# Optimization experiments

Measured on AMD Instinct MI355X. Metric: run time of the kernel, lower is better.

The kernel has to match this reference:

```python
import jax, jax.numpy as jnp
import numpy as np

B, S, H = 16, 4096, 1024

def setup_inputs() -> dict:
    key = jax.random.key(0)
    k1, k2, k3 = jax.random.split(key, 3)
    lstm_output = jax.random.normal(k1, (B, S, H), dtype=jnp.float32)
    # nn.Linear(H, H): weight [H, H] (out, in), bias [H]
    W = jax.random.normal(k2, (H, H), dtype=jnp.float32) * (1.0 / np.sqrt(H))
    b = jax.random.normal(k3, (H,), dtype=jnp.float32) * 0.01
    return {"lstm_output": lstm_output, "W": W, "b": b}

def reference(lstm_output, W, b):
    # energy = tanh(x @ W^T + b)  [B, S, H]
    energy = jnp.tanh(jnp.einsum('bsh,oh->bso', lstm_output, W) + b)
    # softmax over the sequence dim (dim=1), per hidden channel
    scores = jax.nn.softmax(energy, axis=1)
    # weighted-sum pooling over sequence -> [B, H]
    context = jnp.sum(scores * lstm_output, axis=1)
    return context
```

## Files before the change

### kernel.cpp

```cpp
#include <hip/hip_runtime.h>
#include <hip/hip_bf16.h>

#define Bsz  16
#define Sdim 4096
#define Hdim 1024
#define Mtot (Bsz * Sdim)
#define Kdim Hdim
#define Ndim Hdim

#define BM2 256
#define BN2 256
#define BK2 32
#define MT2 (Mtot / BM2)
#define NT2 (Ndim / BN2)
#define NKT2 (Kdim / BK2)

#define BM 128
#define BN 128
#define BK 32
#define MT (Mtot / BM)
#define NT (Ndim / BN)
#define NKT (Kdim / BK)

typedef short s16x8 __attribute__((ext_vector_type(8)));
typedef float f32x4 __attribute__((ext_vector_type(4)));

__device__ __forceinline__ unsigned short f2bf(float f) {
  __hip_bfloat16 h = __float2bfloat16(f);
  unsigned short u;
  __builtin_memcpy(&u, &h, 2);
  return u;
}
__device__ __forceinline__ float bf2f(unsigned short u) {
  __hip_bfloat16 h;
  __builtin_memcpy(&h, &u, 2);
  return __bfloat162float(h);
}
__device__ __forceinline__ s16x8 cvt8(float4 u, float4 v) {
  s16x8 r;
  r[0] = (short)f2bf(u.x); r[1] = (short)f2bf(u.y);
  r[2] = (short)f2bf(u.z); r[3] = (short)f2bf(u.w);
  r[4] = (short)f2bf(v.x); r[5] = (short)f2bf(v.y);
  r[6] = (short)f2bf(v.z); r[7] = (short)f2bf(v.w);
  return r;
}

__device__ __forceinline__ void gload_lds16(const unsigned short* g, unsigned short* l) {
  __builtin_amdgcn_global_load_lds(
      (const __attribute__((address_space(1))) unsigned int*)g,
      (__attribute__((address_space(3))) unsigned int*)l,
      16, 0, 0);
}

__global__ __launch_bounds__(256) void xconv_kernel(const float* __restrict__ X,
                                                    unsigned short* __restrict__ Xb) {
  size_t i = (size_t)blockIdx.x * 256 + threadIdx.x;
  float4 u = reinterpret_cast<const float4*>(X)[2 * i];
  float4 v = reinterpret_cast<const float4*>(X)[2 * i + 1];
  reinterpret_cast<s16x8*>(Xb)[i] = cvt8(u, v);
}

__global__ __launch_bounds__(256) void wconv_kernel(const float* __restrict__ W,
                                                    unsigned short* __restrict__ Wb) {
  int i = blockIdx.x * 256 + threadIdx.x;
  float4 v = reinterpret_cast<const float4*>(W)[i];
  ushort4 o;
  o.x = f2bf(v.x); o.y = f2bf(v.y); o.z = f2bf(v.z); o.w = f2bf(v.w);
  reinterpret_cast<ushort4*>(Wb)[i] = o;
}

__global__ __launch_bounds__(512, 2) void attn_main(
    const unsigned short* __restrict__ Xb,
    const unsigned short* __restrict__ Wb,
    const float* __restrict__ bias,
    float* __restrict__ lpart,
    float* __restrict__ cpart) {
  __shared__ unsigned short Asl[4][BM2 * BK2];
  __shared__ unsigned short Bsl[4][BN2 * BK2];
  __shared__ float red[2][2][BN2];

  int bid = blockIdx.x;
  int swz = (bid & 7) * (MT2 * NT2 / 8) + (bid >> 3);
  const int mt = swz >> 2;
  const int nt = swz & 3;
  const int m0 = mt * BM2;
  const int n0 = nt * BN2;

  const int tid  = threadIdx.x;
  const int l    = tid & 63;
  const int w    = tid >> 6;
  const int wm   = w >> 2;
  const int wn   = w & 3;
  const int lr   = l & 15;
  const int lk   = l >> 4;

  f32x4 acc[8][4];
#pragma unroll
  for (int i = 0; i < 8; i++)
#pragma unroll
    for (int j = 0; j < 4; j++) acc[i][j] = (f32x4){0.f, 0.f, 0.f, 0.f};

  const int srow = w * 16 + (l >> 2);
  const int scol = (((l & 3) ^ ((l >> 3) & 3)) << 3);
  const unsigned short* srcA0 = Xb + (size_t)(m0 + srow) * Kdim + scol;
  const unsigned short* srcA1 = srcA0 + (size_t)128 * Kdim;
  const unsigned short* srcB0 = Wb + (size_t)(n0 + srow) * Kdim + scol;
  const unsigned short* srcB1 = srcB0 + (size_t)128 * Kdim;

  int offA[8], offB[4];
#pragma unroll
  for (int mr = 0; mr < 8; mr++) {
    const int r = wm * 128 + mr * 16 + lr;
    offA[mr] = r * BK2 + ((lk * 8) ^ (((r >> 1) & 3) << 3));
  }
#pragma unroll
  for (int n = 0; n < 4; n++) {
    const int rn = wn * 64 + n * 16 + lr;
    offB[n] = rn * BK2 + ((lk * 8) ^ (((rn >> 1) & 3) << 3));
  }

#pragma unroll
  for (int u = 0; u < 3; ++u) {
    unsigned short* dA = &Asl[u][w * 512];
    unsigned short* dB = &Bsl[u][w * 512];
    gload_lds16(srcA0 + u * BK2, dA);
    gload_lds16(srcA1 + u * BK2, dA + 4096);
    gload_lds16(srcB0 + u * BK2, dB);
    gload_lds16(srcB1 + u * BK2, dB + 4096);
  }

  for (int t = 0; t < NKT2; ++t) {
    if (t < NKT2 - 2)       asm volatile("s_waitcnt vmcnt(8)" ::: "memory");
    else if (t == NKT2 - 2) asm volatile("s_waitcnt vmcnt(4)" ::: "memory");
    else                    asm volatile("s_waitcnt vmcnt(0)" ::: "memory");
    __builtin_amdgcn_s_barrier();

    const int tp = t + 3;
    if (tp < NKT2) {
      unsigned short* dA = &Asl[tp & 3][w * 512];
      unsigned short* dB = &Bsl[tp & 3][w * 512];
      gload_lds16(srcA0 + tp * BK2, dA);
      gload_lds16(srcA1 + tp * BK2, dA + 4096);
      gload_lds16(srcB0 + tp * BK2, dB);
      gload_lds16(srcB1 + tp * BK2, dB + 4096);
    }
    asm volatile("" ::: "memory");

    const unsigned short* As = Asl[t & 3];
    const unsigned short* Bs = Bsl[t & 3];
    s16x8 af[8], bf[4];
#pragma unroll
    for (int j = 0; j < 8; ++j) af[j] = *(const s16x8*)&As[offA[j]];
#pragma unroll
    for (int n = 0; n < 4; ++n) bf[n] = *(const s16x8*)&Bs[offB[n]];
#pragma unroll
    for (int j = 0; j < 8; ++j)
#pragma unroll
      for (int n = 0; n < 4; ++n)
        acc[j][n] = __builtin_amdgcn_mfma_f32_16x16x32_bf16(af[j], bf[n], acc[j][n], 0, 0, 0);
  }

  float lsum[4], csum[4];
#pragma unroll
  for (int nr = 0; nr < 4; nr++) {
    const int o = n0 + wn * 64 + nr * 16 + lr;
    const float bv = bias[o];
    float lacc = 0.f, cacc = 0.f;
#pragma unroll
    for (int mr = 0; mr < 8; mr++) {
      const int sr = m0 + wm * 128 + mr * 16 + lk * 4;
#pragma unroll
      for (int r = 0; r < 4; r++) {
        float e  = acc[mr][nr][r] + bv;
        float t  = __expf(2.f * e);
        float th = 1.f - __fdividef(2.f, t + 1.f);
        float sc = __expf(th);
        float xv = bf2f(Xb[(size_t)(sr + r) * Kdim + o]);
        lacc += sc;
        cacc += sc * xv;
      }
    }
    lacc += __shfl_xor(lacc, 16); lacc += __shfl_xor(lacc, 32);
    cacc += __shfl_xor(cacc, 16); cacc += __shfl_xor(cacc, 32);
    lsum[nr] = lacc; csum[nr] = cacc;
  }

  if (lk == 0) {
#pragma unroll
    for (int nr = 0; nr < 4; nr++) {
      red[wm][0][wn * 64 + nr * 16 + lr] = lsum[nr];
      red[wm][1][wn * 64 + nr * 16 + lr] = csum[nr];
    }
  }
  __syncthreads();
  if (tid < BN2) {
    float L = red[0][0][tid] + red[1][0][tid];
    float C = red[0][1][tid] + red[1][1][tid];
    lpart[(size_t)mt * Ndim + n0 + tid] = L;
    cpart[(size_t)mt * Ndim + n0 + tid] = C;
  }
}

__global__ __launch_bounds__(256) void attn_main_fb(
    const float* __restrict__ X, const unsigned short* __restrict__ Wb,
    const float* __restrict__ bias, float* __restrict__ lpart, float* __restrict__ cpart) {
  __shared__ unsigned short Al[BM * BK];
  __shared__ unsigned short Bl[BN * BK];
  __shared__ float red[2][2][BN];
  int bid = blockIdx.x;
  int swz = (bid & 7) * (MT * NT / 8) + (bid >> 3);
  int mt = swz >> 3, nt = swz & 7;
  const int m0 = mt * BM, n0 = nt * BN;
  const int tid = threadIdx.x, lane = tid & 63, wave = tid >> 6;
  const int wm = wave >> 1, wn = wave & 1, lr = lane & 15, lk = lane >> 4;
  f32x4 acc[4][4];
#pragma unroll
  for (int i = 0; i < 4; i++)
#pragma unroll
    for (int j = 0; j < 4; j++) acc[i][j] = (f32x4){0.f, 0.f, 0.f, 0.f};
  const int srow_st = tid >> 1, scol_st = (tid & 1) * 16;
  const float*          Ag = X  + (size_t)(m0 + srow_st) * Kdim + scol_st;
  const unsigned short* Bg = Wb + (size_t)(n0 + srow_st) * Kdim + scol_st;
  float4 a0 = *(const float4*)(Ag + 0), a1 = *(const float4*)(Ag + 4);
  float4 a2 = *(const float4*)(Ag + 8), a3 = *(const float4*)(Ag + 12);
  s16x8 b0 = *(const s16x8*)(Bg + 0), b1 = *(const s16x8*)(Bg + 8);
  for (int kt = 0; kt < NKT; ++kt) {
    __syncthreads();
    *(s16x8*)&Al[srow_st * BK + scol_st]     = cvt8(a0, a1);
    *(s16x8*)&Al[srow_st * BK + scol_st + 8] = cvt8(a2, a3);
    *(s16x8*)&Bl[srow_st * BK + scol_st]     = b0;
    *(s16x8*)&Bl[srow_st * BK + scol_st + 8] = b1;
    __syncthreads();
    if (kt + 1 < NKT) {
      const float* ap = Ag + (kt + 1) * BK;
      a0 = *(const float4*)(ap);     a1 = *(const float4*)(ap + 4);
      a2 = *(const float4*)(ap + 8); a3 = *(const float4*)(ap + 12);
      const unsigned short* bp = Bg + (kt + 1) * BK;
      b0 = *(const s16x8*)(bp);      b1 = *(const s16x8*)(bp + 8);
    }
    s16x8 af[4], bfr[4];
#pragma unroll
    for (int mr = 0; mr < 4; mr++)
      af[mr] = *(const s16x8*)&Al[(wm * 64 + mr * 16 + lr) * BK + lk * 8];
#pragma unroll
    for (int nr = 0; nr < 4; nr++)
      bfr[nr] = *(const s16x8*)&Bl[(wn * 64 + nr * 16 + lr) * BK + lk * 8];
#pragma unroll
    for (int mr = 0; mr < 4; mr++)
#pragma unroll
      for (int nr = 0; nr < 4; nr++)
        acc[mr][nr] = __builtin_amdgcn_mfma_f32_16x16x32_bf16(af[mr], bfr[nr], acc[mr][nr], 0, 0, 0);
  }
  float lsum[4], csum[4];
#pragma unroll
  for (int nr = 0; nr < 4; nr++) {
    const int o = n0 + wn * 64 + nr * 16 + lr;
    const float bv = bias[o];
    float lacc = 0.f, cacc = 0.f;
#pragma unroll
    for (int mr = 0; mr < 4; mr++) {
      const int sr = m0 + wm * 64 + mr * 16 + lk * 4;
#pragma unroll
      for (int r = 0; r < 4; r++) {
        float e  = acc[mr][nr][r] + bv;
        float t  = __expf(2.f * e);
        float th = 1.f - __fdividef(2.f, t + 1.f);
        float sc = __expf(th);
        float xv = X[(size_t)(sr + r) * Kdim + o];
        lacc += sc; cacc += sc * xv;
      }
    }
    lacc += __shfl_xor(lacc, 16); lacc += __shfl_xor(lacc, 32);
    cacc += __shfl_xor(cacc, 16); cacc += __shfl_xor(cacc, 32);
    lsum[nr] = lacc; csum[nr] = cacc;
  }
  if (lk == 0) {
#pragma unroll
    for (int nr = 0; nr < 4; nr++) {
      red[wm][0][wn * 64 + nr * 16 + lr] = lsum[nr];
      red[wm][1][wn * 64 + nr * 16 + lr] = csum[nr];
    }
  }
  __syncthreads();
  if (tid < BN) {
    float L = red[0][0][tid] + red[1][0][tid];
    float C = red[0][1][tid] + red[1][1][tid];
    lpart[(size_t)mt * Ndim + n0 + tid] = L;
    cpart[(size_t)mt * Ndim + n0 + tid] = C;
  }
}

__global__ __launch_bounds__(256) void finalize_kernel(const float* __restrict__ lpart,
                                                       const float* __restrict__ cpart,
                                                       float* __restrict__ out, int chunks) {
  int i = blockIdx.x * 256 + threadIdx.x;
  int b = i >> 10, o = i & 1023;
  float L = 0.f, C = 0.f;
  for (int sc = 0; sc < chunks; ++sc) {
    size_t idx = (size_t)(b * chunks + sc) * Ndim + o;
    L += lpart[idx];
    C += cpart[idx];
  }
  out[i] = C / L;
}

extern "C" void kernel_launch(void* const* d_in, const int* in_sizes, int n_in,
                              void* d_out, int out_size, void* d_ws, size_t ws_size,
                              hipStream_t stream) {
  const float* X    = (const float*)d_in[0];
  const float* W    = (const float*)d_in[1];
  const float* bias = (const float*)d_in[2];
  float* out = (float*)d_out;

  const size_t xb_bytes = (size_t)Mtot * Kdim * 2;
  const size_t wb_bytes = (size_t)Ndim * Kdim * 2;
  const size_t lp_bytes = (size_t)MT * Ndim * 4;
  const size_t need = xb_bytes + wb_bytes + 2 * lp_bytes;

  if (ws_size >= need) {
    unsigned short* Xb = (unsigned short*)d_ws;
    unsigned short* Wb = (unsigned short*)((char*)d_ws + xb_bytes);
    float* lpart = (float*)((char*)d_ws + xb_bytes + wb_bytes);
    float* cpart = lpart + (size_t)MT2 * Ndim;
    xconv_kernel<<<dim3(Mtot * (Kdim / 8) / 256), dim3(256), 0, stream>>>(X, Xb);
    wconv_kernel<<<dim3(Ndim * Kdim / 1024), dim3(256), 0, stream>>>(W, Wb);
    attn_main<<<dim3(MT2 * NT2), dim3(512), 0, stream>>>(Xb, Wb, bias, lpart, cpart);
    finalize_kernel<<<dim3(Bsz * Hdim / 256), dim3(256), 0, stream>>>(lpart, cpart, out,
                                                                      Sdim / BM2);
  } else {
    unsigned short* Wb = (unsigned short*)d_ws;
    float* lpart = (float*)((char*)d_ws + wb_bytes);
    float* cpart = lpart + (size_t)MT * Ndim;
    wconv_kernel<<<dim3(Ndim * Kdim / 1024), dim3(256), 0, stream>>>(W, Wb);
    attn_main_fb<<<dim3(MT * NT), dim3(256), 0, stream>>>(X, Wb, bias, lpart, cpart);
    finalize_kernel<<<dim3(Bsz * Hdim / 256), dim3(256), 0, stream>>>(lpart, cpart, out,
                                                                      Sdim / BM);
  }
}
```

Measured before the change: 280.4 us.

## Restructure GEMM main loop into 4-phase ping-pong with interleaved staging and setprio

Replaces the 4-stage BK=32 LDS ring with a double-buffered BK=64 scheme split into two K-halves. Each iteration runs four sub-phases, and each sub-phase issues one chunk of global-to-LDS prefetch for the next tile. Barriers and s_setprio bracket the MFMA bursts so loads and math from different waves overlap. This is meant to raise MFMA utilization and cut the serialization between waits and math, but it adds more barriers per K-step and relies on fragile hand-tuned vmcnt counts.

```diff
diff --git a/kernel.cpp b/kernel.cpp
--- a/kernel.cpp
+++ b/kernel.cpp
@@ -10,10 +10,10 @@
 
 #define BM2 256
 #define BN2 256
-#define BK2 32
+#define BK64 64
 #define MT2 (Mtot / BM2)
 #define NT2 (Ndim / BN2)
-#define NKT2 (Kdim / BK2)
+#define NKT64 (Kdim / BK64)
 
 #define BM 128
 #define BN 128
@@ -75,8 +75,8 @@
     const float* __restrict__ bias,
     float* __restrict__ lpart,
     float* __restrict__ cpart) {
-  __shared__ unsigned short Asl[4][BM2 * BK2];
-  __shared__ unsigned short Bsl[4][BN2 * BK2];
+  __shared__ unsigned short Asl[2][2][BM2 * 32];
+  __shared__ unsigned short Bsl[2][2][BN2 * 32];
   __shared__ float red[2][2][BN2];
 
   int bid = blockIdx.x;
@@ -107,57 +107,118 @@
   const unsigned short* srcB0 = Wb + (size_t)(n0 + srow) * Kdim + scol;
   const unsigned short* srcB1 = srcB0 + (size_t)128 * Kdim;
 
-  int offA[8], offB[4];
-#pragma unroll
-  for (int mr = 0; mr < 8; mr++) {
-    const int r = wm * 128 + mr * 16 + lr;
-    offA[mr] = r * BK2 + ((lk * 8) ^ (((r >> 1) & 3) << 3));
-  }
+  int offA[2][4], offB[4];
+#pragma unroll
+  for (int mh = 0; mh < 2; mh++)
+#pragma unroll
+    for (int j = 0; j < 4; j++) {
+      const int r = wm * 128 + mh * 64 + j * 16 + lr;
+      offA[mh][j] = r * 32 + ((lk ^ ((r >> 1) & 3)) << 3);
+    }
 #pragma unroll
   for (int n = 0; n < 4; n++) {
     const int rn = wn * 64 + n * 16 + lr;
-    offB[n] = rn * BK2 + ((lk * 8) ^ (((rn >> 1) & 3) << 3));
-  }
-
-#pragma unroll
-  for (int u = 0; u < 3; ++u) {
-    unsigned short* dA = &Asl[u][w * 512];
-    unsigned short* dB = &Bsl[u][w * 512];
-    gload_lds16(srcA0 + u * BK2, dA);
-    gload_lds16(srcA1 + u * BK2, dA + 4096);
-    gload_lds16(srcB0 + u * BK2, dB);
-    gload_lds16(srcB1 + u * BK2, dB + 4096);
-  }
-
-  for (int t = 0; t < NKT2; ++t) {
-    if (t < NKT2 - 2)       asm volatile("s_waitcnt vmcnt(8)" ::: "memory");
-    else if (t == NKT2 - 2) asm volatile("s_waitcnt vmcnt(4)" ::: "memory");
-    else                    asm volatile("s_waitcnt vmcnt(0)" ::: "memory");
-    __builtin_amdgcn_s_barrier();
-
-    const int tp = t + 3;
-    if (tp < NKT2) {
-      unsigned short* dA = &Asl[tp & 3][w * 512];
-      unsigned short* dB = &Bsl[tp & 3][w * 512];
-      gload_lds16(srcA0 + tp * BK2, dA);
-      gload_lds16(srcA1 + tp * BK2, dA + 4096);
-      gload_lds16(srcB0 + tp * BK2, dB);
-      gload_lds16(srcB1 + tp * BK2, dB + 4096);
-    }
-    asm volatile("" ::: "memory");
-
-    const unsigned short* As = Asl[t & 3];
-    const unsigned short* Bs = Bsl[t & 3];
-    s16x8 af[8], bf[4];
-#pragma unroll
-    for (int j = 0; j < 8; ++j) af[j] = *(const s16x8*)&As[offA[j]];
-#pragma unroll
-    for (int n = 0; n < 4; ++n) bf[n] = *(const s16x8*)&Bs[offB[n]];
-#pragma unroll
-    for (int j = 0; j < 8; ++j)
+    offB[n] = rn * 32 + ((lk ^ ((rn >> 1) & 3)) << 3);
+  }
+
+#define STAGE_A(tp, kh) do {                                            \
+    unsigned short* d = &Asl[(tp) & 1][kh][w * 512];                    \
+    const unsigned short* g = srcA0 + (size_t)(tp) * 64 + (kh) * 32;    \
+    gload_lds16(g, d);                                                  \
+    gload_lds16(g + (size_t)128 * Kdim, d + 4096);                      \
+  } while (0)
+#define STAGE_B(tp, kh) do {                                            \
+    unsigned short* d = &Bsl[(tp) & 1][kh][w * 512];                    \
+    const unsigned short* g = srcB0 + (size_t)(tp) * 64 + (kh) * 32;    \
+    gload_lds16(g, d);                                                  \
+    gload_lds16(g + (size_t)128 * Kdim, d + 4096);                      \
+  } while (0)
+
+#define MID_BARRIER() do {                                   \
+    asm volatile("" ::: "memory");                           \
+    __builtin_amdgcn_s_barrier();                            \
+    asm volatile("s_waitcnt lgkmcnt(0)" ::: "memory");       \
+    __builtin_amdgcn_sched_barrier(0);                       \
+  } while (0)
+#define END_BARRIER() do {                                   \
+    asm volatile("" ::: "memory");                           \
+    __builtin_amdgcn_s_barrier();                            \
+  } while (0)
+
+  STAGE_A(0, 0); STAGE_B(0, 0); STAGE_A(0, 1); STAGE_B(0, 1);
+  asm volatile("s_waitcnt vmcnt(4)" ::: "memory");
+  END_BARRIER();
+
+  s16x8 bf0[4], bf1[4];
+
+  for (int t = 0; t < NKT64; ++t) {
+    const int s = t & 1;
+    const unsigned short* As0 = Asl[s][0];
+    const unsigned short* As1 = Asl[s][1];
+    const unsigned short* Bs0 = Bsl[s][0];
+    const unsigned short* Bs1 = Bsl[s][1];
+    const int tp = t + 1;
+    const bool more = (tp < NKT64);
+    s16x8 af[4];
+
+#pragma unroll
+    for (int j = 0; j < 4; ++j) af[j] = *(const s16x8*)&As0[offA[0][j]];
+#pragma unroll
+    for (int n = 0; n < 4; ++n) bf0[n] = *(const s16x8*)&Bs0[offB[n]];
+    if (more) STAGE_A(tp, 0);
+    MID_BARRIER();
+    __builtin_amdgcn_s_setprio(1);
+#pragma unroll
+    for (int j = 0; j < 4; ++j)
 #pragma unroll
       for (int n = 0; n < 4; ++n)
-        acc[j][n] = __builtin_amdgcn_mfma_f32_16x16x32_bf16(af[j], bf[n], acc[j][n], 0, 0, 0);
+        acc[j][n] = __builtin_amdgcn_mfma_f32_16x16x32_bf16(af[j], bf0[n], acc[j][n], 0, 0, 0);
+    __builtin_amdgcn_s_setprio(0);
+    if (more) asm volatile("s_waitcnt vmcnt(2)" ::: "memory");
+    else      asm volatile("s_waitcnt vmcnt(0)" ::: "memory");
+    END_BARRIER();
+
+#pragma unroll
+    for (int j = 0; j < 4; ++j) af[j] = *(const s16x8*)&As1[offA[0][j]];
+#pragma unroll
+    for (int n = 0; n < 4; ++n) bf1[n] = *(const s16x8*)&Bs1[offB[n]];
+    if (more) STAGE_B(tp, 0);
+    MID_BARRIER();
+    __builtin_amdgcn_s_setprio(1);
+#pragma unroll
+    for (int j = 0; j < 4; ++j)
+#pragma unroll
+      for (int n = 0; n < 4; ++n)
+        acc[j][n] = __builtin_amdgcn_mfma_f32_16x16x32_bf16(af[j], bf1[n], acc[j][n], 0, 0, 0);
+    __builtin_amdgcn_s_setprio(0);
+    END_BARRIER();
+
+#pragma unroll
+    for (int j = 0; j < 4; ++j) af[j] = *(const s16x8*)&As0[offA[1][j]];
+    if (more) STAGE_A(tp, 1);
+    MID_BARRIER();
+    __builtin_amdgcn_s_setprio(1);
+#pragma unroll
+    for (int j = 0; j < 4; ++j)
+#pragma unroll
+      for (int n = 0; n < 4; ++n)
+        acc[4 + j][n] = __builtin_amdgcn_mfma_f32_16x16x32_bf16(af[j], bf0[n], acc[4 + j][n], 0, 0, 0);
+    __builtin_amdgcn_s_setprio(0);
+    END_BARRIER();
+
+#pragma unroll
+    for (int j = 0; j < 4; ++j) af[j] = *(const s16x8*)&As1[offA[1][j]];
+    if (more) STAGE_B(tp, 1);
+    MID_BARRIER();
+    __builtin_amdgcn_s_setprio(1);
+#pragma unroll
+    for (int j = 0; j < 4; ++j)
+#pragma unroll
+      for (int n = 0; n < 4; ++n)
+        acc[4 + j][n] = __builtin_amdgcn_mfma_f32_16x16x32_bf16(af[j], bf1[n], acc[4 + j][n], 0, 0, 0);
+    __builtin_amdgcn_s_setprio(0);
+    if (more) asm volatile("s_waitcnt vmcnt(4)" ::: "memory");
+    END_BARRIER();
   }
 
   float lsum[4], csum[4];
@@ -167,11 +228,11 @@
     const float bv = bias[o];
     float lacc = 0.f, cacc = 0.f;
 #pragma unroll
-    for (int mr = 0; mr < 8; mr++) {
-      const int sr = m0 + wm * 128 + mr * 16 + lk * 4;
+    for (int m8 = 0; m8 < 8; m8++) {
+      const int sr = m0 + wm * 128 + (m8 >> 2) * 64 + (m8 & 3) * 16 + lk * 4;
 #pragma unroll
       for (int r = 0; r < 4; r++) {
-        float e  = acc[mr][nr][r] + bv;
+        float e  = acc[m8][nr][r] + bv;
         float t  = __expf(2.f * e);
         float th = 1.f - __fdividef(2.f, t + 1.f);
         float sc = __expf(th);
```

New measurement: 244.9 us. -12.7%, faster.

## Restructure GEMM main loop into ping-pong BK=64 stages with interleaved loads and MFMA

Applied to the files above, without the earlier changes.

Replaces the 4-stage BK=32 LDS ring with even/odd BK=64 double buffers. Each iteration is split into eight sub-phases that alternate LDS fragment reads, single global-to-LDS stage loads and 16-MFMA blocks, separated by barriers and wrapped in s_setprio. The aim is finer overlap of memory traffic with matrix math and better latency hiding, in the style of hipBLASLt 8-wave schedules. In exchange it adds many more barriers per K-step and uses a new XOR swizzle and fragment ordering, which the epilogue's row mapping has to match.

```diff
diff --git a/kernel.cpp b/kernel.cpp
--- a/kernel.cpp
+++ b/kernel.cpp
@@ -10,10 +10,10 @@
 
 #define BM2 256
 #define BN2 256
-#define BK2 32
 #define MT2 (Mtot / BM2)
 #define NT2 (Ndim / BN2)
-#define NKT2 (Kdim / BK2)
+#define NKT64 (Kdim / 64)
+#define NITER (NKT64 / 2)
 
 #define BM 128
 #define BN 128
@@ -75,8 +75,10 @@
     const float* __restrict__ bias,
     float* __restrict__ lpart,
     float* __restrict__ cpart) {
-  __shared__ unsigned short Asl[4][BM2 * BK2];
-  __shared__ unsigned short Bsl[4][BN2 * BK2];
+  __shared__ unsigned short Aev[2 * 8192];
+  __shared__ unsigned short Aod[2 * 8192];
+  __shared__ unsigned short Bev[2 * 8192];
+  __shared__ unsigned short Bod[2 * 8192];
   __shared__ float red[2][2][BN2];
 
   int bid = blockIdx.x;
@@ -86,13 +88,13 @@
   const int m0 = mt * BM2;
   const int n0 = nt * BN2;
 
-  const int tid  = threadIdx.x;
-  const int l    = tid & 63;
-  const int w    = tid >> 6;
-  const int wm   = w >> 2;
-  const int wn   = w & 3;
-  const int lr   = l & 15;
-  const int lk   = l >> 4;
+  const int tid = threadIdx.x;
+  const int l   = tid & 63;
+  const int w   = tid >> 6;
+  const int wm  = w >> 2;
+  const int wn  = w & 3;
+  const int lr  = l & 15;
+  const int lk  = l >> 4;
 
   f32x4 acc[8][4];
 #pragma unroll
@@ -100,64 +102,114 @@
 #pragma unroll
     for (int j = 0; j < 4; j++) acc[i][j] = (f32x4){0.f, 0.f, 0.f, 0.f};
 
-  const int srow = w * 16 + (l >> 2);
-  const int scol = (((l & 3) ^ ((l >> 3) & 3)) << 3);
-  const unsigned short* srcA0 = Xb + (size_t)(m0 + srow) * Kdim + scol;
-  const unsigned short* srcA1 = srcA0 + (size_t)128 * Kdim;
-  const unsigned short* srcB0 = Wb + (size_t)(n0 + srow) * Kdim + scol;
-  const unsigned short* srcB1 = srcB0 + (size_t)128 * Kdim;
-
-  int offA[8], offB[4];
-#pragma unroll
-  for (int mr = 0; mr < 8; mr++) {
-    const int r = wm * 128 + mr * 16 + lr;
-    offA[mr] = r * BK2 + ((lk * 8) ^ (((r >> 1) & 3) << 3));
-  }
-#pragma unroll
-  for (int n = 0; n < 4; n++) {
-    const int rn = wn * 64 + n * 16 + lr;
-    offB[n] = rn * BK2 + ((lk * 8) ^ (((rn >> 1) & 3) << 3));
-  }
-
-#pragma unroll
-  for (int u = 0; u < 3; ++u) {
-    unsigned short* dA = &Asl[u][w * 512];
-    unsigned short* dB = &Bsl[u][w * 512];
-    gload_lds16(srcA0 + u * BK2, dA);
-    gload_lds16(srcA1 + u * BK2, dA + 4096);
-    gload_lds16(srcB0 + u * BK2, dB);
-    gload_lds16(srcB1 + u * BK2, dB + 4096);
-  }
-
-  for (int t = 0; t < NKT2; ++t) {
-    if (t < NKT2 - 2)       asm volatile("s_waitcnt vmcnt(8)" ::: "memory");
-    else if (t == NKT2 - 2) asm volatile("s_waitcnt vmcnt(4)" ::: "memory");
-    else                    asm volatile("s_waitcnt vmcnt(0)" ::: "memory");
-    __builtin_amdgcn_s_barrier();
-
-    const int tp = t + 3;
-    if (tp < NKT2) {
-      unsigned short* dA = &Asl[tp & 3][w * 512];
-      unsigned short* dB = &Bsl[tp & 3][w * 512];
-      gload_lds16(srcA0 + tp * BK2, dA);
-      gload_lds16(srcA1 + tp * BK2, dA + 4096);
-      gload_lds16(srcB0 + tp * BK2, dB);
-      gload_lds16(srcB1 + tp * BK2, dB + 4096);
-    }
-    asm volatile("" ::: "memory");
-
-    const unsigned short* As = Asl[t & 3];
-    const unsigned short* Bs = Bsl[t & 3];
-    s16x8 af[8], bf[4];
-#pragma unroll
-    for (int j = 0; j < 8; ++j) af[j] = *(const s16x8*)&As[offA[j]];
-#pragma unroll
-    for (int n = 0; n < 4; ++n) bf[n] = *(const s16x8*)&Bs[offB[n]];
-#pragma unroll
-    for (int j = 0; j < 8; ++j)
-#pragma unroll
-      for (int n = 0; n < 4; ++n)
-        acc[j][n] = __builtin_amdgcn_mfma_f32_16x16x32_bf16(af[j], bf[n], acc[j][n], 0, 0, 0);
+  const int xk0 = ((lk ^ (lr & 7)) << 3);
+  const int xk1 = (((4 | lk) ^ (lr & 7)) << 3);
+
+  const unsigned short* AevW = Aev + wm * 8192;
+  const unsigned short* AodW = Aod + wm * 8192;
+  const unsigned short* BevW = Bev + (wn >> 1) * 8192;
+  const unsigned short* BodW = Bod + (wn >> 1) * 8192;
+
+  const int srowU = tid >> 3;
+  const int scolE = (((tid & 7) ^ ((tid >> 3) & 7)) << 3);
+  const unsigned short* sA0 = Xb + (size_t)(m0 + srowU) * Kdim + scolE;
+  const unsigned short* sA1 = Xb + (size_t)(m0 + 128 + srowU) * Kdim + scolE;
+  const unsigned short* sB0 = Wb + (size_t)(n0 + srowU) * Kdim + scolE;
+  const unsigned short* sB1 = Wb + (size_t)(n0 + 128 + srowU) * Kdim + scolE;
+
+#define STG(arrbase, src, tile) do {                              \
+    unsigned short* d_ = (arrbase) + w * 512;                     \
+    const unsigned short* g_ = (src) + (size_t)(tile) * 64;       \
+    gload_lds16(g_, d_);                                          \
+    gload_lds16(g_ + 65536, d_ + 4096);                           \
+  } while (0)
+
+#define RD_A(base, MH) do {                                              \
+    _Pragma("unroll")                                                    \
+    for (int mf = 0; mf < 4; ++mf) {                                     \
+      const unsigned short* p_ = (base) + ((MH)*64 + mf*16 + lr) * 64;   \
+      af[mf][0] = *(const s16x8*)(p_ + xk0);                             \
+      af[mf][1] = *(const s16x8*)(p_ + xk1);                             \
+    } } while (0)
+
+#define RD_B(base, NH, BF) do {                                          \
+    _Pragma("unroll")                                                    \
+    for (int nf = 0; nf < 2; ++nf) {                                     \
+      const unsigned short* p_ =                                         \
+          (base) + ((wn & 1) * 64 + (NH)*32 + nf*16 + lr) * 64;          \
+      BF[nf][0] = *(const s16x8*)(p_ + xk0);                             \
+      BF[nf][1] = *(const s16x8*)(p_ + xk1);                             \
+    } } while (0)
+
+#define MFMA16(MH, NH, BF) do {                                          \
+    __builtin_amdgcn_s_setprio(1);                                       \
+    _Pragma("unroll")                                                    \
+    for (int kk = 0; kk < 2; ++kk)                                       \
+      _Pragma("unroll")                                                  \
+      for (int mf = 0; mf < 4; ++mf)                                     \
+        _Pragma("unroll")                                                \
+        for (int nf = 0; nf < 2; ++nf)                                   \
+          acc[(MH)*4 + mf][(NH)*2 + nf] =                                \
+              __builtin_amdgcn_mfma_f32_16x16x32_bf16(                   \
+                  af[mf][kk], BF[nf][kk], acc[(MH)*4 + mf][(NH)*2 + nf], \
+                  0, 0, 0);                                              \
+    __builtin_amdgcn_s_setprio(0);                                       \
+  } while (0)
+
+#define BAR() do {                                   \
+    asm volatile("" ::: "memory");                   \
+    __builtin_amdgcn_s_barrier();                    \
+    asm volatile("" ::: "memory");                   \
+  } while (0)
+#define VM2() asm volatile("s_waitcnt vmcnt(2)" ::: "memory")
+#define VM0() asm volatile("s_waitcnt vmcnt(0)" ::: "memory")
+
+  STG(Aev + 0,    sA0, 0);
+  STG(Aev + 8192, sA1, 0);
+  STG(Bev + 0,    sB0, 0);
+  STG(Bev + 8192, sB1, 0);
+  STG(Aod + 0,    sA0, 1);
+  VM2();
+  BAR();
+
+  for (int u = 0; u < NITER; ++u) {
+    const int t1o = 2 * u + 1;
+    const int t2  = 2 * u + 2;
+    const int t3  = 2 * u + 3;
+    const bool st = (u < NITER - 1);
+    s16x8 af[4][2], bf0[2][2], bf1[2][2];
+
+    RD_A(AevW, 0); RD_B(BevW, 0, bf0);
+    STG(Aod + 8192, sA1, t1o);
+    BAR(); MFMA16(0, 0, bf0); BAR();
+
+    RD_B(BevW, 1, bf1);
+    STG(Bod + 0, sB0, t1o);
+    BAR(); MFMA16(0, 1, bf1); BAR();
+
+    RD_A(AevW, 1);
+    STG(Bod + 8192, sB1, t1o);
+    BAR(); MFMA16(1, 1, bf1); BAR();
+
+    if (st) STG(Aev + 0, sA0, t2);
+    if (st) VM2(); else VM0();
+    BAR(); MFMA16(1, 0, bf0); BAR();
+
+    RD_A(AodW, 0); RD_B(BodW, 0, bf0);
+    if (st) STG(Aev + 8192, sA1, t2);
+    BAR(); MFMA16(0, 0, bf0); BAR();
+
+    RD_B(BodW, 1, bf1);
+    if (st) STG(Bev + 0, sB0, t2);
+    BAR(); MFMA16(0, 1, bf1); BAR();
+
+    RD_A(AodW, 1);
+    if (st) STG(Bev + 8192, sB1, t2);
+    BAR(); MFMA16(1, 1, bf1); BAR();
+
+    if (st) STG(Aod + 0, sA0, t3);
+    if (st) VM2();
+    BAR(); MFMA16(1, 0, bf0); BAR();
   }
 
   float lsum[4], csum[4];
@@ -167,11 +219,11 @@
     const float bv = bias[o];
     float lacc = 0.f, cacc = 0.f;
 #pragma unroll
-    for (int mr = 0; mr < 8; mr++) {
-      const int sr = m0 + wm * 128 + mr * 16 + lk * 4;
+    for (int m8 = 0; m8 < 8; m8++) {
+      const int sr = m0 + wm * 128 + (m8 >> 2) * 64 + (m8 & 3) * 16 + lk * 4;
 #pragma unroll
       for (int r = 0; r < 4; r++) {
-        float e  = acc[mr][nr][r] + bv;
+        float e  = acc[m8][nr][r] + bv;
         float t  = __expf(2.f * e);
         float th = 1.f - __fdividef(2.f, t + 1.f);
         float sc = __expf(th);
```

Result: faster. 250.8 us (-10.5%).
